# Optimization experiments

Hardware: AMD Instinct MI355X
Metric: run time of the kernel (lower is better)

The kernel has to match this reference:

```python
import jax, jax.numpy as jnp
import numpy as np

B, S, H, A, I = 64, 512, 1024, 1024, 1024


def setup_inputs() -> dict:
    key = jax.random.key(0)
    ks = jax.random.split(key, 12)
    s = lambda fan_in: 1.0 / np.sqrt(fan_in)
    return {
        "encoded": jax.random.normal(ks[0], (B, S, H), jnp.float32),
        "inputs": jax.random.normal(ks[1], (B, I), jnp.float32),
        "states": jax.random.normal(ks[2], (B, H), jnp.float32),
        # attention params
        "W_enc": jax.random.uniform(ks[3], (H, A), jnp.float32, -s(H), s(H)),
        "b_enc": jnp.zeros((A,), jnp.float32),
        "W_dec": jax.random.uniform(ks[4], (H, A), jnp.float32, -s(H), s(H)),
        "b_dec": jnp.zeros((A,), jnp.float32),
        "w_out": jax.random.uniform(ks[5], (A, 1), jnp.float32, -s(A), s(A)),
        "b_out": jnp.zeros((1,), jnp.float32),
        # GRU cell params (input size = I + H)
        "W_ih": jax.random.uniform(ks[6], (3 * H, I + H), jnp.float32, -s(H), s(H)),
        "W_hh": jax.random.uniform(ks[7], (3 * H, H), jnp.float32, -s(H), s(H)),
        "b_ih": jax.random.uniform(ks[8], (3 * H,), jnp.float32, -s(H), s(H)),
        "b_hh": jax.random.uniform(ks[9], (3 * H,), jnp.float32, -s(H), s(H)),
    }


def reference(encoded, inputs, states, W_enc, b_enc, W_dec, b_dec, w_out, b_out,
              W_ih, W_hh, b_ih, b_hh):
    # setup_memory: project encoder states  [B,S,H] @ [H,A] -> [B,S,A]
    enc_proj = jnp.einsum("bsh,ha->bsa", encoded, W_enc) + b_enc
    # project decoder state and broadcast over S
    dec_proj = states @ W_dec + b_dec                      # [B,A]
    projected = enc_proj + dec_proj[:, None, :]            # [B,S,A]
    scores = jnp.tanh(projected) @ w_out + b_out           # [B,S,1]
    weights = jax.nn.softmax(scores, axis=1)               # [B,S,1]
    attention = jnp.sum(encoded * weights, axis=1)         # [B,H]
    # GRU cell on concatenated input
    x = jnp.concatenate([inputs, attention], axis=1)       # [B,I+H]
    gi = x @ W_ih.T + b_ih                                 # [B,3H]
    gh = states @ W_hh.T + b_hh                            # [B,3H]
    i_r, i_z, i_n = jnp.split(gi, 3, axis=1)
    h_r, h_z, h_n = jnp.split(gh, 3, axis=1)
    r = jax.nn.sigmoid(i_r + h_r)
    z = jax.nn.sigmoid(i_z + h_z)
    n = jnp.tanh(i_n + r * h_n)
    return (1.0 - z) * n + z * states                      # [B,H]
```

## Files before the change

### kernel.cpp

```cpp
#include <hip/hip_runtime.h>
#include <stdint.h>

typedef __bf16 bf16x8 __attribute__((ext_vector_type(8)));
typedef float f32x4 __attribute__((ext_vector_type(4)));

#define LOG2E 1.4426950408889634f
#define LSTR 32

__device__ __forceinline__ unsigned short f2bf(float f) {
  unsigned int x = __builtin_bit_cast(unsigned int, f);
  x += 0x7FFFu + ((x >> 16) & 1u);
  return (unsigned short)(x >> 16);
}
__device__ __forceinline__ float bflo(unsigned int u) {
  return __builtin_bit_cast(float, u << 16);
}
__device__ __forceinline__ float bfhi(unsigned int u) {
  return __builtin_bit_cast(float, u & 0xffff0000u);
}
__device__ __forceinline__ float tanh_fast(float x) {
  float cx = fminf(fmaxf(x, -15.f), 15.f);
  float e = __builtin_amdgcn_exp2f(cx * (2.f * LOG2E));
  return (e - 1.f) * __builtin_amdgcn_rcpf(e + 1.f);
}
__device__ __forceinline__ float sigmoid_fast(float x) {
  float cx = fminf(fmaxf(x, -30.f), 30.f);
  float e = __builtin_amdgcn_exp2f(cx * LOG2E);
  return e * __builtin_amdgcn_rcpf(e + 1.f);
}
__device__ __forceinline__ ushort4 cvt4(const float4 f) {
  return make_ushort4(f2bf(f.x), f2bf(f.y), f2bf(f.z), f2bf(f.w));
}

__device__ __forceinline__ void gl_lds16(const unsigned short* g,
                                         const unsigned short* lds_base) {
  __builtin_amdgcn_global_load_lds(
      (const __attribute__((address_space(1))) unsigned int*)(uintptr_t)g,
      (__attribute__((address_space(3))) unsigned int*)(unsigned int)(uintptr_t)lds_base,
      16, 0, 0);
}

__global__ __launch_bounds__(256) void k_prep(
    const float* __restrict__ W_enc, unsigned short* __restrict__ Wt,
    const float* __restrict__ states, const float* __restrict__ W_dec,
    const float* __restrict__ b_dec, const float* __restrict__ b_enc,
    float* __restrict__ dvec, float4* __restrict__ zbase,
    const float* __restrict__ enc, unsigned short* __restrict__ encb) {
  __shared__ unsigned short tile[64][65];
  __shared__ float red[256];
  const int bid = blockIdx.x;
  const int tid = threadIdx.x;
  if (bid < 256) {
    const int bx = bid & 15, by = bid >> 4;
    const int x = tid & 63, y0 = tid >> 6;
#pragma unroll
    for (int i = y0; i < 64; i += 4)
      tile[i][x] = f2bf(W_enc[(size_t)(by * 64 + i) * 1024 + bx * 64 + x]);
    __syncthreads();
#pragma unroll
    for (int i = y0; i < 64; i += 4)
      Wt[(size_t)(bx * 64 + i) * 1024 + by * 64 + x] = tile[x][i];
  } else if (bid < 768) {
    const int bb = bid - 256;
    const int b = bb >> 3;
    const int a0 = (bb & 7) * 128;
    const int a = tid & 127, half = tid >> 7;
    const float* sp = states + (size_t)b * 1024;
    const float* wp = W_dec + a0 + a;
    float acc = 0.f;
    const int kb = half * 512;
#pragma unroll 8
    for (int k = kb; k < kb + 512; ++k)
      acc += sp[k] * wp[(size_t)k * 1024];
    red[tid] = acc;
    __syncthreads();
    if (tid < 128) {
      float v = red[tid] + red[tid + 128];
      dvec[(size_t)b * 1024 + a0 + tid] = v + b_dec[a0 + tid] + b_enc[a0 + tid];
    }
  } else if (bid < 1248) {
    const float4 z = {0.f, 0.f, 0.f, 0.f};
    zbase[(size_t)(bid - 768) * 256 + tid] = z;
  } else {
    const size_t i = ((size_t)(bid - 1248) * 256 + tid) * 8;
    const float4 f0 = *(const float4*)(enc + i);
    const float4 f1 = *(const float4*)(enc + i + 4);
    *(ushort4*)(encb + i) = cvt4(f0);
    *(ushort4*)(encb + i + 4) = cvt4(f1);
  }
}

__global__ __launch_bounds__(256, 3) void k_scores_bf16(
    const unsigned short* __restrict__ encb,
    const unsigned short* __restrict__ Wt,
    const float* __restrict__ dvec,
    const float* __restrict__ w_out,
    float* __restrict__ scores) {
  __shared__ alignas(16) unsigned short lds[2][8192];
  __shared__ float sc[128];

  const int tid = threadIdx.x;
  const int wave = tid >> 6, lane = tid & 63;
  const int l15 = lane & 15, quad = lane >> 4;
  const int mt = blockIdx.x >> 3;
  const int nt = blockIdx.x & 7;
  const int row0 = mt * 128;
  const int b = row0 >> 9;
  const int wm = (wave >> 1) * 64, wn = (wave & 1) * 64;
  const int srow = lane >> 2;
  const int fsw = ((lane >> 2) & 3) ^ ((lane >> 4) & 3);
  const int skoff = (((lane & 3) ^ fsw) * 8);
  const int rchunk = ((quad ^ ((l15 & 3) ^ ((l15 >> 2) & 3))) * 8);

  if (tid < 128) sc[tid] = 0.f;

  const unsigned short* gsrc[4];
#pragma unroll
  for (int s = 0; s < 4; ++s) {
    const int g = wave * 4 + s;
    gsrc[s] = (g < 8)
        ? encb + (size_t)(row0 + g * 16 + srow) * 1024 + skoff
        : Wt + (size_t)(nt * 128 + (g - 8) * 16 + srow) * 1024 + skoff;
  }

  const f32x4 vz = {0.f, 0.f, 0.f, 0.f};
  f32x4 acc[4][4];
#pragma unroll
  for (int i = 0; i < 4; ++i)
#pragma unroll
    for (int j = 0; j < 4; ++j) acc[i][j] = vz;

#define STAGE(BUF, KK)                                              \
  do {                                                              \
    _Pragma("unroll") for (int s = 0; s < 4; ++s)                   \
        gl_lds16(gsrc[s] + (KK), &lds[BUF][(wave * 4 + s) * 512]);  \
  } while (0)

#define COMPUTE(BUF)                                                          \
  do {                                                                        \
    bf16x8 af[4], bg[4];                                                      \
    _Pragma("unroll") for (int i = 0; i < 4; ++i)                             \
        af[i] = *(const bf16x8*)(&lds[BUF][(wm + i * 16 + l15) * LSTR + rchunk]); \
    _Pragma("unroll") for (int j = 0; j < 4; ++j)                             \
        bg[j] = *(const bf16x8*)(&lds[BUF][4096 + (wn + j * 16 + l15) * LSTR + rchunk]); \
    _Pragma("unroll") for (int i = 0; i < 4; ++i)                             \
      _Pragma("unroll") for (int j = 0; j < 4; ++j)                           \
          acc[i][j] = __builtin_amdgcn_mfma_f32_16x16x32_bf16(af[i], bg[j],   \
                                                              acc[i][j], 0, 0, 0); \
  } while (0)

  STAGE(0, 0);
  __syncthreads();

#pragma unroll 1
  for (int k0 = 0; k0 < 1024; k0 += 64) {
    STAGE(1, k0 + 32);
    COMPUTE(0);
    __syncthreads();
    if (k0 + 64 < 1024) { STAGE(0, k0 + 64); }
    COMPUTE(1);
    __syncthreads();
  }
#undef STAGE
#undef COMPUTE

  float p[4][4];
#pragma unroll
  for (int i = 0; i < 4; ++i)
#pragma unroll
    for (int r = 0; r < 4; ++r) p[i][r] = 0.f;
#pragma unroll
  for (int j = 0; j < 4; ++j) {
    const int a = nt * 128 + wn + j * 16 + l15;
    const float dv = dvec[(size_t)b * 1024 + a];
    const float wo = w_out[a];
#pragma unroll
    for (int i = 0; i < 4; ++i)
#pragma unroll
      for (int r = 0; r < 4; ++r)
        p[i][r] += tanh_fast(acc[i][j][r] + dv) * wo;
  }
#pragma unroll
  for (int i = 0; i < 4; ++i)
#pragma unroll
    for (int r = 0; r < 4; ++r) {
      float v = p[i][r];
      v += __shfl_xor(v, 1);
      v += __shfl_xor(v, 2);
      v += __shfl_xor(v, 4);
      v += __shfl_xor(v, 8);
      if (l15 == 0) atomicAdd(&sc[wm + i * 16 + quad * 4 + r], v);
    }
  __syncthreads();
  if (tid < 128)
    atomicAdd(&scores[(size_t)b * 512 + (row0 & 511) + tid], sc[tid]);
}

__global__ __launch_bounds__(256) void k_scores_f32(
    const float* __restrict__ enc, const unsigned short* __restrict__ Wt,
    const float* __restrict__ dvec, const float* __restrict__ w_out,
    float* __restrict__ scores) {
  __shared__ alignas(16) unsigned short lA[128 * LSTR];
  __shared__ alignas(16) unsigned short lB[128 * LSTR];
  __shared__ float sc[128];
  const int tid = threadIdx.x;
  const int wave = tid >> 6, lane = tid & 63;
  const int l15 = lane & 15, quad = lane >> 4;
  const int mt = blockIdx.x >> 2, nh = blockIdx.x & 3;
  const int row0 = mt * 128, b = row0 >> 9;
  const int wm = (wave >> 1) * 64, wn = (wave & 1) * 64;
  const int srow = lane >> 2, skoff = (lane & 3) * 8;
  if (tid < 128) sc[tid] = 0.f;
  const f32x4 vz = {0.f, 0.f, 0.f, 0.f};
#pragma unroll 1
  for (int t2 = 0; t2 < 2; ++t2) {
    const int nt = nh * 2 + t2;
    f32x4 acc[4][4];
#pragma unroll
    for (int i = 0; i < 4; ++i)
#pragma unroll
      for (int j = 0; j < 4; ++j) acc[i][j] = vz;
#pragma unroll 1
    for (int k0 = 0; k0 < 1024; k0 += 32) {
      ushort4 sa[2][2];
      uint4 vb[2];
#pragma unroll
      for (int rr = 0; rr < 2; ++rr) {
        const int r = wave * 2 + rr;
        const float* ap = enc + (size_t)(row0 + r * 16 + srow) * 1024 + k0 + skoff;
        sa[rr][0] = cvt4(*(const float4*)ap);
        sa[rr][1] = cvt4(*(const float4*)(ap + 4));
        vb[rr] = *(const uint4*)(Wt + (size_t)(nt * 128 + r * 16 + srow) * 1024 + k0 + skoff);
      }
      __syncthreads();
#pragma unroll
      for (int rr = 0; rr < 2; ++rr) {
        const int r = wave * 2 + rr;
        *(ushort4*)(lA + (r * 16 + srow) * LSTR + skoff) = sa[rr][0];
        *(ushort4*)(lA + (r * 16 + srow) * LSTR + skoff + 4) = sa[rr][1];
        *(uint4*)(lB + (r * 16 + srow) * LSTR + skoff) = vb[rr];
      }
      __syncthreads();
      bf16x8 af[4], bg[4];
#pragma unroll
      for (int i = 0; i < 4; ++i)
        af[i] = *(const bf16x8*)(lA + (wm + i * 16 + l15) * LSTR + quad * 8);
#pragma unroll
      for (int j = 0; j < 4; ++j)
        bg[j] = *(const bf16x8*)(lB + (wn + j * 16 + l15) * LSTR + quad * 8);
#pragma unroll
      for (int i = 0; i < 4; ++i)
#pragma unroll
        for (int j = 0; j < 4; ++j)
          acc[i][j] = __builtin_amdgcn_mfma_f32_16x16x32_bf16(af[i], bg[j],
                                                              acc[i][j], 0, 0, 0);
    }
    float p[4][4];
#pragma unroll
    for (int i = 0; i < 4; ++i)
#pragma unroll
      for (int r = 0; r < 4; ++r) p[i][r] = 0.f;
#pragma unroll
    for (int j = 0; j < 4; ++j) {
      const int a = nt * 128 + wn + j * 16 + l15;
      const float dv = dvec[(size_t)b * 1024 + a];
      const float wo = w_out[a];
#pragma unroll
      for (int i = 0; i < 4; ++i)
#pragma unroll
        for (int r = 0; r < 4; ++r)
          p[i][r] += tanh_fast(acc[i][j][r] + dv) * wo;
    }
#pragma unroll
    for (int i = 0; i < 4; ++i)
#pragma unroll
      for (int r = 0; r < 4; ++r) {
        float v = p[i][r];
        v += __shfl_xor(v, 1);
        v += __shfl_xor(v, 2);
        v += __shfl_xor(v, 4);
        v += __shfl_xor(v, 8);
        if (l15 == 0) atomicAdd(&sc[wm + i * 16 + quad * 4 + r], v);
      }
  }
  __syncthreads();
  if (tid < 128)
    atomicAdd(&scores[(size_t)b * 512 + (row0 & 511) + tid], sc[tid]);
}

template <bool ABF16>
__global__ __launch_bounds__(256) void k_attn(const void* __restrict__ encv,
                                              const float* __restrict__ scores,
                                              float* __restrict__ att) {
  const int b = blockIdx.x >> 2;
  const int scn = blockIdx.x & 3;
  const int tid = threadIdx.x;
  __shared__ float w[512];
  __shared__ float redm[4], reds[4];

  const float s0 = scores[(size_t)b * 512 + tid];
  const float s1 = scores[(size_t)b * 512 + 256 + tid];
  float m = fmaxf(s0, s1);
#pragma unroll
  for (int off = 32; off; off >>= 1) m = fmaxf(m, __shfl_xor(m, off));
  const int wv = tid >> 6;
  if ((tid & 63) == 0) redm[wv] = m;
  __syncthreads();
  m = fmaxf(fmaxf(redm[0], redm[1]), fmaxf(redm[2], redm[3]));
  const float e0 = __builtin_amdgcn_exp2f((s0 - m) * LOG2E);
  const float e1 = __builtin_amdgcn_exp2f((s1 - m) * LOG2E);
  float sum = e0 + e1;
#pragma unroll
  for (int off = 32; off; off >>= 1) sum += __shfl_xor(sum, off);
  if ((tid & 63) == 0) reds[wv] = sum;
  __syncthreads();
  sum = reds[0] + reds[1] + reds[2] + reds[3];
  const float inv = 1.f / sum;
  w[tid] = e0 * inv;
  w[tid + 256] = e1 * inv;
  __syncthreads();

  const int h0 = (tid & 127) * 8;
  const int sh = tid >> 7;
  float a[8];
#pragma unroll
  for (int i = 0; i < 8; ++i) a[i] = 0.f;
  const size_t base = ((size_t)(b * 512 + scn * 128 + sh)) * 1024 + h0;
#pragma unroll 4
  for (int i = 0; i < 64; ++i) {
    const float ws_ = w[scn * 128 + sh + 2 * i];
    if constexpr (ABF16) {
      const uint4 v = *(const uint4*)((const unsigned short*)encv + base + (size_t)(2 * i) * 1024);
      a[0] += ws_ * bflo(v.x); a[1] += ws_ * bfhi(v.x);
      a[2] += ws_ * bflo(v.y); a[3] += ws_ * bfhi(v.y);
      a[4] += ws_ * bflo(v.z); a[5] += ws_ * bfhi(v.z);
      a[6] += ws_ * bflo(v.w); a[7] += ws_ * bfhi(v.w);
    } else {
      const float* ep = (const float*)encv + base + (size_t)(2 * i) * 1024;
      const float4 v0 = *(const float4*)ep;
      const float4 v1 = *(const float4*)(ep + 4);
      a[0] += ws_ * v0.x; a[1] += ws_ * v0.y;
      a[2] += ws_ * v0.z; a[3] += ws_ * v0.w;
      a[4] += ws_ * v1.x; a[5] += ws_ * v1.y;
      a[6] += ws_ * v1.z; a[7] += ws_ * v1.w;
    }
  }
#pragma unroll
  for (int i = 0; i < 8; ++i)
    atomicAdd(&att[(size_t)b * 1024 + h0 + i], a[i]);
}

__global__ __launch_bounds__(256) void k_gru_gemm(
    const float* __restrict__ xin,
    const float* __restrict__ att,
    const float* __restrict__ states,
    const float* __restrict__ W_ih,
    const float* __restrict__ W_hh,
    float* __restrict__ gbuf) {
  const int tid = threadIdx.x;
  const int wave = tid >> 6, lane = tid & 63;
  const int l15 = lane & 15, quad = lane >> 4;
  const int kk = blockIdx.x & 3;
  const int rest = blockIdx.x >> 2;
  const bool is_gh = rest >= 48;
  const int nt = is_gh ? rest - 48 : rest;
  const int n0 = nt * 64;
  const int KT = is_gh ? 1024 : 2048;
  const int Kh = KT >> 2;
  const int kbase = kk * Kh;
  const float* W = is_gh ? W_hh : W_ih;
  float* outp = gbuf + (is_gh ? (size_t)64 * 3072 : 0);

  __shared__ alignas(16) unsigned short lA[64 * LSTR];
  __shared__ alignas(16) unsigned short lB[64 * LSTR];

  const f32x4 vz = {0.f, 0.f, 0.f, 0.f};
  f32x4 acc[2][2];
  acc[0][0] = vz; acc[0][1] = vz; acc[1][0] = vz; acc[1][1] = vz;

  const int arow = tid >> 2;
  const int achunk = (tid & 3) * 8;
  const int fswG = ((tid >> 2) & 3) ^ ((tid >> 4) & 3);
  const int wchunk = (((tid & 3) ^ fswG) * 8);
  const int rchunkG = ((quad ^ ((l15 & 3) ^ ((l15 >> 2) & 3))) * 8);
  const int wm2 = (wave >> 1) * 32, wn2 = (wave & 1) * 32;

  float4 ra0, ra1, rb0, rb1;
  auto LOADK = [&](int kg0) {
    const int kg = kg0 + achunk;
    const float* ap = is_gh ? (states + (size_t)arow * 1024 + kg)
                    : (kg < 1024 ? (xin + (size_t)arow * 1024 + kg)
                                 : (att + (size_t)arow * 1024 + (kg - 1024)));
    ra0 = *(const float4*)ap;
    ra1 = *(const float4*)(ap + 4);
    const float* wp = W + (size_t)(n0 + arow) * KT + kg;
    rb0 = *(const float4*)wp;
    rb1 = *(const float4*)(wp + 4);
  };
  LOADK(kbase);

#pragma unroll 1
  for (int k0 = 0; k0 < Kh; k0 += 32) {
    __syncthreads();
    *(ushort4*)(lA + arow * LSTR + wchunk) = cvt4(ra0);
    *(ushort4*)(lA + arow * LSTR + wchunk + 4) = cvt4(ra1);
    *(ushort4*)(lB + arow * LSTR + wchunk) = cvt4(rb0);
    *(ushort4*)(lB + arow * LSTR + wchunk + 4) = cvt4(rb1);
    __syncthreads();
    if (k0 + 32 < Kh) LOADK(kbase + k0 + 32);
    bf16x8 af[2], bg[2];
#pragma unroll
    for (int i = 0; i < 2; ++i)
      af[i] = *(const bf16x8*)(lA + (wm2 + i * 16 + l15) * LSTR + rchunkG);
#pragma unroll
    for (int j = 0; j < 2; ++j)
      bg[j] = *(const bf16x8*)(lB + (wn2 + j * 16 + l15) * LSTR + rchunkG);
#pragma unroll
    for (int i = 0; i < 2; ++i)
#pragma unroll
      for (int j = 0; j < 2; ++j)
        acc[i][j] = __builtin_amdgcn_mfma_f32_16x16x32_bf16(af[i], bg[j],
                                                            acc[i][j], 0, 0, 0);
  }
#pragma unroll
  for (int i = 0; i < 2; ++i)
#pragma unroll
    for (int j = 0; j < 2; ++j)
#pragma unroll
      for (int r = 0; r < 4; ++r) {
        const int m = wm2 + i * 16 + quad * 4 + r;
        const int n = n0 + wn2 + j * 16 + l15;
        atomicAdd(&outp[(size_t)m * 3072 + n], acc[i][j][r]);
      }
}

__global__ void k_gate(const float* __restrict__ gbuf,
                       const float* __restrict__ states,
                       const float* __restrict__ b_ih,
                       const float* __restrict__ b_hh,
                       float* __restrict__ outp) {
  const int idx = blockIdx.x * 256 + threadIdx.x;
  const int b = idx >> 10, h = idx & 1023;
  const float* gi = gbuf + (size_t)b * 3072;
  const float* gh = gbuf + (size_t)64 * 3072 + (size_t)b * 3072;
  const float ir = gi[h] + b_ih[h];
  const float iz = gi[1024 + h] + b_ih[1024 + h];
  const float in_ = gi[2048 + h] + b_ih[2048 + h];
  const float hr = gh[h] + b_hh[h];
  const float hz = gh[1024 + h] + b_hh[1024 + h];
  const float hn = gh[2048 + h] + b_hh[2048 + h];
  const float r = sigmoid_fast(ir + hr);
  const float z = sigmoid_fast(iz + hz);
  const float n = tanh_fast(in_ + r * hn);
  const float hp = states[idx];
  outp[idx] = (1.f - z) * n + z * hp;
}

extern "C" void kernel_launch(void* const* d_in, const int* in_sizes, int n_in,
                              void* d_out, int out_size, void* d_ws, size_t ws_size,
                              hipStream_t stream) {
  const float* enc    = (const float*)d_in[0];
  const float* xin    = (const float*)d_in[1];
  const float* states = (const float*)d_in[2];
  const float* W_enc  = (const float*)d_in[3];
  const float* b_enc  = (const float*)d_in[4];
  const float* W_dec  = (const float*)d_in[5];
  const float* b_dec  = (const float*)d_in[6];
  const float* w_out  = (const float*)d_in[7];
  const float* W_ih   = (const float*)d_in[9];
  const float* W_hh   = (const float*)d_in[10];
  const float* b_ih   = (const float*)d_in[11];
  const float* b_hh   = (const float*)d_in[12];
  float* out = (float*)d_out;

  const size_t ENC_BF16_BYTES = (size_t)32768 * 1024 * 2;
  const bool use_bf16 = ws_size >= ENC_BF16_BYTES + (8u << 20);

  char* ws = (char*)d_ws;
  unsigned short* encb = (unsigned short*)ws;
  char* base = ws + (use_bf16 ? ENC_BF16_BYTES : 0);
  unsigned short* Wt = (unsigned short*)base;
  float* dvec    = (float*)(base + 2097152);
  float* scoresb = (float*)(base + 2097152 + 262144);
  float* att     = (float*)(base + 2097152 + 262144 + 131072);
  float* gbuf    = (float*)(base + 2097152 + 262144 + 131072 + 262144);

  const int prep_grid = use_bf16 ? 17632 : 1248;
  k_prep<<<prep_grid, 256, 0, stream>>>(W_enc, Wt, states, W_dec, b_dec, b_enc,
                                        dvec, (float4*)scoresb, enc, encb);
  if (use_bf16) {
    k_scores_bf16<<<2048, 256, 0, stream>>>(encb, Wt, dvec, w_out, scoresb);
    k_attn<true><<<256, 256, 0, stream>>>(encb, scoresb, att);
  } else {
    k_scores_f32<<<1024, 256, 0, stream>>>(enc, Wt, dvec, w_out, scoresb);
    k_attn<false><<<256, 256, 0, stream>>>(enc, scoresb, att);
  }
  k_gru_gemm<<<384, 256, 0, stream>>>(xin, att, states, W_ih, W_hh, gbuf);
  k_gate<<<256, 256, 0, stream>>>(gbuf, states, b_ih, b_hh, out);
}
```

Before: 411.9 us.

## Fuse fp32-to-bf16 encoder conversion into scores GEMM A-tile staging

Drops the separate pass that converted the whole encoder tensor to bf16 in workspace. The scores GEMM now loads fp32 encoder rows into registers, converts them, and writes swizzled bf16 into LDS, while W_enc tiles still arrive by direct global-to-LDS DMA. The loop is restructured into a register-prefetch double buffer with two barriers per 32-wide k-step. Attention now reads fp32 encoder data directly. This removes a 64MB write and re-read, but each of the 8 N-tile blocks re-reads and re-converts fp32 A, doubling A read bytes per GEMM block.

```diff
diff --git a/kernel.cpp b/kernel.cpp
--- a/kernel.cpp
+++ b/kernel.cpp
@@ -3,6 +3,7 @@
 
 typedef __bf16 bf16x8 __attribute__((ext_vector_type(8)));
 typedef float f32x4 __attribute__((ext_vector_type(4)));
+typedef unsigned short u16x8 __attribute__((ext_vector_type(8)));
 
 #define LOG2E 1.4426950408889634f
 #define LSTR 32
@@ -11,12 +12,6 @@
   unsigned int x = __builtin_bit_cast(unsigned int, f);
   x += 0x7FFFu + ((x >> 16) & 1u);
   return (unsigned short)(x >> 16);
-}
-__device__ __forceinline__ float bflo(unsigned int u) {
-  return __builtin_bit_cast(float, u << 16);
-}
-__device__ __forceinline__ float bfhi(unsigned int u) {
-  return __builtin_bit_cast(float, u & 0xffff0000u);
 }
 __device__ __forceinline__ float tanh_fast(float x) {
   float cx = fminf(fmaxf(x, -15.f), 15.f);
@@ -44,8 +39,7 @@
     const float* __restrict__ W_enc, unsigned short* __restrict__ Wt,
     const float* __restrict__ states, const float* __restrict__ W_dec,
     const float* __restrict__ b_dec, const float* __restrict__ b_enc,
-    float* __restrict__ dvec, float4* __restrict__ zbase,
-    const float* __restrict__ enc, unsigned short* __restrict__ encb) {
+    float* __restrict__ dvec, float4* __restrict__ zbase) {
   __shared__ unsigned short tile[64][65];
   __shared__ float red[256];
   const int bid = blockIdx.x;
@@ -78,20 +72,14 @@
       float v = red[tid] + red[tid + 128];
       dvec[(size_t)b * 1024 + a0 + tid] = v + b_dec[a0 + tid] + b_enc[a0 + tid];
     }
-  } else if (bid < 1248) {
+  } else {
     const float4 z = {0.f, 0.f, 0.f, 0.f};
     zbase[(size_t)(bid - 768) * 256 + tid] = z;
-  } else {
-    const size_t i = ((size_t)(bid - 1248) * 256 + tid) * 8;
-    const float4 f0 = *(const float4*)(enc + i);
-    const float4 f1 = *(const float4*)(enc + i + 4);
-    *(ushort4*)(encb + i) = cvt4(f0);
-    *(ushort4*)(encb + i + 4) = cvt4(f1);
-  }
-}
-
-__global__ __launch_bounds__(256, 3) void k_scores_bf16(
-    const unsigned short* __restrict__ encb,
+  }
+}
+
+__global__ __launch_bounds__(256, 3) void k_scores(
+    const float* __restrict__ enc,
     const unsigned short* __restrict__ Wt,
     const float* __restrict__ dvec,
     const float* __restrict__ w_out,
@@ -107,21 +95,26 @@
   const int row0 = mt * 128;
   const int b = row0 >> 9;
   const int wm = (wave >> 1) * 64, wn = (wave & 1) * 64;
+
   const int srow = lane >> 2;
   const int fsw = ((lane >> 2) & 3) ^ ((lane >> 4) & 3);
   const int skoff = (((lane & 3) ^ fsw) * 8);
+  const unsigned short* gB0 =
+      Wt + (size_t)(nt * 128 + (wave * 2 + 0) * 16 + srow) * 1024 + skoff;
+  const unsigned short* gB1 =
+      Wt + (size_t)(nt * 128 + (wave * 2 + 1) * 16 + srow) * 1024 + skoff;
+
+  const int ar = tid & 127;
+  const int akb = (tid >> 7) * 16;
+  const int kc0 = (tid >> 7) * 2;
+  const int fA = (ar & 3) ^ ((ar >> 2) & 3);
+  const int ws0 = ((kc0 ^ fA) * 8);
+  const int ws1 = (((kc0 + 1) ^ fA) * 8);
+  const float* gA = enc + (size_t)(row0 + ar) * 1024 + akb;
+
   const int rchunk = ((quad ^ ((l15 & 3) ^ ((l15 >> 2) & 3))) * 8);
 
   if (tid < 128) sc[tid] = 0.f;
-
-  const unsigned short* gsrc[4];
-#pragma unroll
-  for (int s = 0; s < 4; ++s) {
-    const int g = wave * 4 + s;
-    gsrc[s] = (g < 8)
-        ? encb + (size_t)(row0 + g * 16 + srow) * 1024 + skoff
-        : Wt + (size_t)(nt * 128 + (g - 8) * 16 + srow) * 1024 + skoff;
-  }
 
   const f32x4 vz = {0.f, 0.f, 0.f, 0.f};
   f32x4 acc[4][4];
@@ -130,39 +123,55 @@
 #pragma unroll
     for (int j = 0; j < 4; ++j) acc[i][j] = vz;
 
-#define STAGE(BUF, KK)                                              \
-  do {                                                              \
-    _Pragma("unroll") for (int s = 0; s < 4; ++s)                   \
-        gl_lds16(gsrc[s] + (KK), &lds[BUF][(wave * 4 + s) * 512]);  \
-  } while (0)
-
-#define COMPUTE(BUF)                                                          \
-  do {                                                                        \
-    bf16x8 af[4], bg[4];                                                      \
-    _Pragma("unroll") for (int i = 0; i < 4; ++i)                             \
-        af[i] = *(const bf16x8*)(&lds[BUF][(wm + i * 16 + l15) * LSTR + rchunk]); \
-    _Pragma("unroll") for (int j = 0; j < 4; ++j)                             \
-        bg[j] = *(const bf16x8*)(&lds[BUF][4096 + (wn + j * 16 + l15) * LSTR + rchunk]); \
-    _Pragma("unroll") for (int i = 0; i < 4; ++i)                             \
-      _Pragma("unroll") for (int j = 0; j < 4; ++j)                           \
-          acc[i][j] = __builtin_amdgcn_mfma_f32_16x16x32_bf16(af[i], bg[j],   \
-                                                              acc[i][j], 0, 0, 0); \
-  } while (0)
-
-  STAGE(0, 0);
-  __syncthreads();
-
+  float4 ra0, ra1, ra2, ra3;
+  auto LOADA = [&](int kk) {
+    ra0 = *(const float4*)(gA + kk);
+    ra1 = *(const float4*)(gA + kk + 4);
+    ra2 = *(const float4*)(gA + kk + 8);
+    ra3 = *(const float4*)(gA + kk + 12);
+  };
+  auto DMAB = [&](int bi, int kk) {
+    unsigned short* base = &lds[0][0] + bi * 8192 + 4096;
+    gl_lds16(gB0 + kk, base + (wave * 2 + 0) * 512);
+    gl_lds16(gB1 + kk, base + (wave * 2 + 1) * 512);
+  };
+  auto WRITEA = [&](int bi) {
+    const ushort4 c0 = cvt4(ra0), c1 = cvt4(ra1), c2 = cvt4(ra2), c3 = cvt4(ra3);
+    u16x8 p0 = {c0.x, c0.y, c0.z, c0.w, c1.x, c1.y, c1.z, c1.w};
+    u16x8 p1 = {c2.x, c2.y, c2.z, c2.w, c3.x, c3.y, c3.z, c3.w};
+    unsigned short* base = &lds[0][0] + bi * 8192;
+    *(u16x8*)(base + ar * LSTR + ws0) = p0;
+    *(u16x8*)(base + ar * LSTR + ws1) = p1;
+  };
+  auto COMPUTE = [&](int bi) {
+    const unsigned short* base = &lds[0][0] + bi * 8192;
+    bf16x8 af[4], bg[4];
+#pragma unroll
+    for (int i = 0; i < 4; ++i)
+      af[i] = *(const bf16x8*)(base + (wm + i * 16 + l15) * LSTR + rchunk);
+#pragma unroll
+    for (int j = 0; j < 4; ++j)
+      bg[j] = *(const bf16x8*)(base + 4096 + (wn + j * 16 + l15) * LSTR + rchunk);
+#pragma unroll
+    for (int i = 0; i < 4; ++i)
+#pragma unroll
+      for (int j = 0; j < 4; ++j)
+        acc[i][j] = __builtin_amdgcn_mfma_f32_16x16x32_bf16(af[i], bg[j],
+                                                            acc[i][j], 0, 0, 0);
+  };
+
+  LOADA(0);
+  DMAB(0, 0);
+  int buf = 0;
 #pragma unroll 1
-  for (int k0 = 0; k0 < 1024; k0 += 64) {
-    STAGE(1, k0 + 32);
-    COMPUTE(0);
-    __syncthreads();
-    if (k0 + 64 < 1024) { STAGE(0, k0 + 64); }
-    COMPUTE(1);
-    __syncthreads();
-  }
-#undef STAGE
-#undef COMPUTE
+  for (int t = 0; t < 32; ++t) {
+    __syncthreads();
+    WRITEA(buf);
+    __syncthreads();
+    if (t + 1 < 32) { LOADA((t + 1) * 32); DMAB(buf ^ 1, (t + 1) * 32); }
+    COMPUTE(buf);
+    buf ^= 1;
+  }
 
   float p[4][4];
 #pragma unroll
@@ -196,100 +205,7 @@
     atomicAdd(&scores[(size_t)b * 512 + (row0 & 511) + tid], sc[tid]);
 }
 
-__global__ __launch_bounds__(256) void k_scores_f32(
-    const float* __restrict__ enc, const unsigned short* __restrict__ Wt,
-    const float* __restrict__ dvec, const float* __restrict__ w_out,
-    float* __restrict__ scores) {
-  __shared__ alignas(16) unsigned short lA[128 * LSTR];
-  __shared__ alignas(16) unsigned short lB[128 * LSTR];
-  __shared__ float sc[128];
-  const int tid = threadIdx.x;
-  const int wave = tid >> 6, lane = tid & 63;
-  const int l15 = lane & 15, quad = lane >> 4;
-  const int mt = blockIdx.x >> 2, nh = blockIdx.x & 3;
-  const int row0 = mt * 128, b = row0 >> 9;
-  const int wm = (wave >> 1) * 64, wn = (wave & 1) * 64;
-  const int srow = lane >> 2, skoff = (lane & 3) * 8;
-  if (tid < 128) sc[tid] = 0.f;
-  const f32x4 vz = {0.f, 0.f, 0.f, 0.f};
-#pragma unroll 1
-  for (int t2 = 0; t2 < 2; ++t2) {
-    const int nt = nh * 2 + t2;
-    f32x4 acc[4][4];
-#pragma unroll
-    for (int i = 0; i < 4; ++i)
-#pragma unroll
-      for (int j = 0; j < 4; ++j) acc[i][j] = vz;
-#pragma unroll 1
-    for (int k0 = 0; k0 < 1024; k0 += 32) {
-      ushort4 sa[2][2];
-      uint4 vb[2];
-#pragma unroll
-      for (int rr = 0; rr < 2; ++rr) {
-        const int r = wave * 2 + rr;
-        const float* ap = enc + (size_t)(row0 + r * 16 + srow) * 1024 + k0 + skoff;
-        sa[rr][0] = cvt4(*(const float4*)ap);
-        sa[rr][1] = cvt4(*(const float4*)(ap + 4));
-        vb[rr] = *(const uint4*)(Wt + (size_t)(nt * 128 + r * 16 + srow) * 1024 + k0 + skoff);
-      }
-      __syncthreads();
-#pragma unroll
-      for (int rr = 0; rr < 2; ++rr) {
-        const int r = wave * 2 + rr;
-        *(ushort4*)(lA + (r * 16 + srow) * LSTR + skoff) = sa[rr][0];
-        *(ushort4*)(lA + (r * 16 + srow) * LSTR + skoff + 4) = sa[rr][1];
-        *(uint4*)(lB + (r * 16 + srow) * LSTR + skoff) = vb[rr];
-      }
-      __syncthreads();
-      bf16x8 af[4], bg[4];
-#pragma unroll
-      for (int i = 0; i < 4; ++i)
-        af[i] = *(const bf16x8*)(lA + (wm + i * 16 + l15) * LSTR + quad * 8);
-#pragma unroll
-      for (int j = 0; j < 4; ++j)
-        bg[j] = *(const bf16x8*)(lB + (wn + j * 16 + l15) * LSTR + quad * 8);
-#pragma unroll
-      for (int i = 0; i < 4; ++i)
-#pragma unroll
-        for (int j = 0; j < 4; ++j)
-          acc[i][j] = __builtin_amdgcn_mfma_f32_16x16x32_bf16(af[i], bg[j],
-                                                              acc[i][j], 0, 0, 0);
-    }
-    float p[4][4];
-#pragma unroll
-    for (int i = 0; i < 4; ++i)
-#pragma unroll
-      for (int r = 0; r < 4; ++r) p[i][r] = 0.f;
-#pragma unroll
-    for (int j = 0; j < 4; ++j) {
-      const int a = nt * 128 + wn + j * 16 + l15;
-      const float dv = dvec[(size_t)b * 1024 + a];
-      const float wo = w_out[a];
-#pragma unroll
-      for (int i = 0; i < 4; ++i)
-#pragma unroll
-        for (int r = 0; r < 4; ++r)
-          p[i][r] += tanh_fast(acc[i][j][r] + dv) * wo;
-    }
-#pragma unroll
-    for (int i = 0; i < 4; ++i)
-#pragma unroll
-      for (int r = 0; r < 4; ++r) {
-        float v = p[i][r];
-        v += __shfl_xor(v, 1);
-        v += __shfl_xor(v, 2);
-        v += __shfl_xor(v, 4);
-        v += __shfl_xor(v, 8);
-        if (l15 == 0) atomicAdd(&sc[wm + i * 16 + quad * 4 + r], v);
-      }
-  }
-  __syncthreads();
-  if (tid < 128)
-    atomicAdd(&scores[(size_t)b * 512 + (row0 & 511) + tid], sc[tid]);
-}
-
-template <bool ABF16>
-__global__ __launch_bounds__(256) void k_attn(const void* __restrict__ encv,
+__global__ __launch_bounds__(256) void k_attn(const float* __restrict__ enc,
                                               const float* __restrict__ scores,
                                               float* __restrict__ att) {
   const int b = blockIdx.x >> 2;
@@ -329,21 +245,13 @@
 #pragma unroll 4
   for (int i = 0; i < 64; ++i) {
     const float ws_ = w[scn * 128 + sh + 2 * i];
-    if constexpr (ABF16) {
-      const uint4 v = *(const uint4*)((const unsigned short*)encv + base + (size_t)(2 * i) * 1024);
-      a[0] += ws_ * bflo(v.x); a[1] += ws_ * bfhi(v.x);
-      a[2] += ws_ * bflo(v.y); a[3] += ws_ * bfhi(v.y);
-      a[4] += ws_ * bflo(v.z); a[5] += ws_ * bfhi(v.z);
-      a[6] += ws_ * bflo(v.w); a[7] += ws_ * bfhi(v.w);
-    } else {
-      const float* ep = (const float*)encv + base + (size_t)(2 * i) * 1024;
-      const float4 v0 = *(const float4*)ep;
-      const float4 v1 = *(const float4*)(ep + 4);
-      a[0] += ws_ * v0.x; a[1] += ws_ * v0.y;
-      a[2] += ws_ * v0.z; a[3] += ws_ * v0.w;
-      a[4] += ws_ * v1.x; a[5] += ws_ * v1.y;
-      a[6] += ws_ * v1.z; a[7] += ws_ * v1.w;
-    }
+    const float* ep = enc + base + (size_t)(2 * i) * 1024;
+    const float4 v0 = *(const float4*)ep;
+    const float4 v1 = *(const float4*)(ep + 4);
+    a[0] += ws_ * v0.x; a[1] += ws_ * v0.y;
+    a[2] += ws_ * v0.z; a[3] += ws_ * v0.w;
+    a[4] += ws_ * v1.x; a[5] += ws_ * v1.y;
+    a[6] += ws_ * v1.z; a[7] += ws_ * v1.w;
   }
 #pragma unroll
   for (int i = 0; i < 8; ++i)
@@ -473,28 +381,17 @@
   const float* b_hh   = (const float*)d_in[12];
   float* out = (float*)d_out;
 
-  const size_t ENC_BF16_BYTES = (size_t)32768 * 1024 * 2;
-  const bool use_bf16 = ws_size >= ENC_BF16_BYTES + (8u << 20);
-
-  char* ws = (char*)d_ws;
-  unsigned short* encb = (unsigned short*)ws;
-  char* base = ws + (use_bf16 ? ENC_BF16_BYTES : 0);
+  char* base = (char*)d_ws;
   unsigned short* Wt = (unsigned short*)base;
   float* dvec    = (float*)(base + 2097152);
   float* scoresb = (float*)(base + 2097152 + 262144);
   float* att     = (float*)(base + 2097152 + 262144 + 131072);
   float* gbuf    = (float*)(base + 2097152 + 262144 + 131072 + 262144);
 
-  const int prep_grid = use_bf16 ? 17632 : 1248;
-  k_prep<<<prep_grid, 256, 0, stream>>>(W_enc, Wt, states, W_dec, b_dec, b_enc,
-                                        dvec, (float4*)scoresb, enc, encb);
-  if (use_bf16) {
-    k_scores_bf16<<<2048, 256, 0, stream>>>(encb, Wt, dvec, w_out, scoresb);
-    k_attn<true><<<256, 256, 0, stream>>>(encb, scoresb, att);
-  } else {
-    k_scores_f32<<<1024, 256, 0, stream>>>(enc, Wt, dvec, w_out, scoresb);
-    k_attn<false><<<256, 256, 0, stream>>>(enc, scoresb, att);
-  }
+  k_prep<<<1248, 256, 0, stream>>>(W_enc, Wt, states, W_dec, b_dec, b_enc,
+                                   dvec, (float4*)scoresb);
+  k_scores<<<2048, 256, 0, stream>>>(enc, Wt, dvec, w_out, scoresb);
+  k_attn<<<256, 256, 0, stream>>>(enc, scoresb, att);
   k_gru_gemm<<<384, 256, 0, stream>>>(xin, att, states, W_ih, W_hh, gbuf);
   k_gate<<<256, 256, 0, stream>>>(gbuf, states, b_ih, b_hh, out);
 }
```

Measured after the change: 496.2 us. 20.5% more time.
